# Kernel tuning notes

Measured on AMD Instinct MI355X. Metric: run time of the kernel, lower is better.

Reference implementation:

```python
import jax, jax.numpy as jnp
from jax import lax
import numpy as np

B, S, D_IN = 2048, 512, 5
H, E_DIM, N_EMB, C_CONV = 64, 32, 64, 32
COMMIT = 0.01


def _lstm_params(key, in_dim, hid):
    ks = jax.random.split(key, 4)
    sc = 1.0 / np.sqrt(hid)
    wih = jax.random.uniform(ks[0], (4 * hid, in_dim), minval=-sc, maxval=sc)
    whh = jax.random.uniform(ks[1], (4 * hid, hid), minval=-sc, maxval=sc)
    bih = jax.random.uniform(ks[2], (4 * hid,), minval=-sc, maxval=sc)
    bhh = jax.random.uniform(ks[3], (4 * hid,), minval=-sc, maxval=sc)
    return wih, whh, bih, bhh


def setup_inputs() -> dict:
    key = jax.random.key(0)
    ks = jax.random.split(key, 12)
    inp = {}
    inp['x'] = jax.random.normal(ks[0], (B, S, D_IN), dtype=jnp.float32)
    inp['conv_w'] = jax.random.normal(ks[1], (C_CONV, D_IN, 3)) * 0.2  # OIH
    inp['conv_b'] = jax.random.normal(ks[2], (C_CONV,)) * 0.05
    inp['bn_g'] = jnp.ones((C_CONV,)) + jax.random.normal(ks[3], (C_CONV,)) * 0.05
    inp['bn_b'] = jax.random.normal(ks[4], (C_CONV,)) * 0.05
    inp['bn_m'] = jax.random.normal(ks[5], (C_CONV,)) * 0.1
    inp['bn_v'] = jax.random.uniform(ks[6], (C_CONV,), minval=0.5, maxval=1.5)
    cw = _lstm_params(ks[7], C_CONV, H)
    cw1 = _lstm_params(jax.random.fold_in(ks[7], 1), H, H)
    vw = _lstm_params(ks[8], D_IN, H)
    vw1 = _lstm_params(jax.random.fold_in(ks[8], 1), H, H)
    for pre, p in (('cnn0', cw), ('cnn1', cw1), ('vq0', vw), ('vq1', vw1)):
        inp[pre + '_wih'], inp[pre + '_whh'], inp[pre + '_bih'], inp[pre + '_bhh'] = p
    inp['proj_w'] = jax.random.normal(ks[9], (E_DIM, H)) * (1.0 / np.sqrt(H))
    inp['proj_b'] = jax.random.normal(ks[10], (E_DIM,)) * 0.05
    xav = np.sqrt(6.0 / (N_EMB + E_DIM))
    inp['codebook'] = jax.random.uniform(ks[11], (N_EMB, E_DIM), minval=-xav, maxval=xav)
    return inp


def _lstm_layer(xs, wih, whh, bih, bhh):
    # xs: [S, B, in] -> (ys [S,B,H], h_final [B,H])
    b = xs.shape[1]
    h0 = jnp.zeros((b, H), xs.dtype)
    bias = bih + bhh

    def step(carry, x_t):
        h, c = carry
        gates = x_t @ wih.T + h @ whh.T + bias
        i, f, g, o = jnp.split(gates, 4, axis=-1)
        c = jax.nn.sigmoid(f) * c + jax.nn.sigmoid(i) * jnp.tanh(g)
        h = jax.nn.sigmoid(o) * jnp.tanh(c)
        return (h, c), h

    (h, c), ys = lax.scan(step, (h0, h0), xs)
    return ys, h


def _forward(x, conv_w, conv_b, bn_g, bn_b, bn_m, bn_v,
             cnn0_wih, cnn0_whh, cnn0_bih, cnn0_bhh,
             cnn1_wih, cnn1_whh, cnn1_bih, cnn1_bhh,
             vq0_wih, vq0_whh, vq0_bih, vq0_bhh,
             vq1_wih, vq1_whh, vq1_bih, vq1_bhh,
             proj_w, proj_b, codebook):
    # CNN stream: conv1d(k=3, pad=1) + BN (eval) + ReLU; dropout = identity (eval)
    x_ncw = jnp.transpose(x, (0, 2, 1))  # [B, D_IN, S]
    y = lax.conv_general_dilated(x_ncw, conv_w, (1,), [(1, 1)],
                                 dimension_numbers=('NCH', 'OIH', 'NCH'))
    y = y + conv_b[None, :, None]
    y = (y - bn_m[None, :, None]) * (bn_g / jnp.sqrt(bn_v + 1e-5))[None, :, None] + bn_b[None, :, None]
    y = jax.nn.relu(y)
    y = jnp.transpose(y, (2, 0, 1))  # [S, B, 32] time-major
    ys, _ = _lstm_layer(y, cnn0_wih, cnn0_whh, cnn0_bih, cnn0_bhh)
    _, cnn_features = _lstm_layer(ys, cnn1_wih, cnn1_whh, cnn1_bih, cnn1_bhh)  # [B, H]

    # VQ stream
    xt = jnp.transpose(x, (1, 0, 2))  # [S, B, D_IN]
    ys2, _ = _lstm_layer(xt, vq0_wih, vq0_whh, vq0_bih, vq0_bhh)
    _, vq_hidden = _lstm_layer(ys2, vq1_wih, vq1_whh, vq1_bih, vq1_bhh)  # [B, H]
    vq_proj = vq_hidden @ proj_w.T + proj_b  # [B, E_DIM]

    # Vector quantization
    d = (jnp.sum(vq_proj ** 2, axis=1, keepdims=True)
         + jnp.sum(codebook ** 2, axis=1)
         - 2.0 * vq_proj @ codebook.T)  # [B, N_EMB]
    idx = jnp.argmin(d, axis=1)
    quantized = codebook[idx]  # [B, E_DIM]
    e_loss = jnp.mean((lax.stop_gradient(quantized) - vq_proj) ** 2)
    q_loss = jnp.mean((quantized - lax.stop_gradient(vq_proj)) ** 2)
    vq_loss = q_loss + COMMIT * e_loss
    quantized = vq_proj + lax.stop_gradient(quantized - vq_proj)  # STE
    enc = jax.nn.one_hot(idx, N_EMB, dtype=vq_proj.dtype)
    avg_probs = jnp.mean(enc, axis=0)
    perplexity = jnp.exp(-jnp.sum(avg_probs * jnp.log(avg_probs + 1e-10)))

    combined = jnp.concatenate([cnn_features, quantized], axis=1)  # [B, H+E_DIM]
    return combined, vq_loss, perplexity


def reference(x, conv_w, conv_b, bn_g, bn_b, bn_m, bn_v,
              cnn0_wih, cnn0_whh, cnn0_bih, cnn0_bhh,
              cnn1_wih, cnn1_whh, cnn1_bih, cnn1_bhh,
              vq0_wih, vq0_whh, vq0_bih, vq0_bhh,
              vq1_wih, vq1_whh, vq1_bih, vq1_bhh,
              proj_w, proj_b, codebook):
    combined, vq_loss, perplexity = _forward(
        x, conv_w, conv_b, bn_g, bn_b, bn_m, bn_v,
        cnn0_wih, cnn0_whh, cnn0_bih, cnn0_bhh,
        cnn1_wih, cnn1_whh, cnn1_bih, cnn1_bhh,
        vq0_wih, vq0_whh, vq0_bih, vq0_bhh,
        vq1_wih, vq1_whh, vq1_bih, vq1_bhh,
        proj_w, proj_b, codebook)
    # num_classes=None -> returns (combined, combined, vq_loss, perplexity)
    return combined, combined, vq_loss, perplexity
```

## Files before the change

kernel.cpp:

```cpp
#include <hip/hip_runtime.h>
#include <math.h>
#include <stdint.h>

#define B_TOT 2048
#define SEQ   512
#define DIN   5
#define HID   64
#define EDIM  32
#define NEMB  64
#define BT    16
#define NBLK_STREAM 128
#define COMB  96
#define OUTC  (B_TOT*COMB)

typedef __attribute__((ext_vector_type(8))) _Float16 half8;
typedef __attribute__((ext_vector_type(4))) float float4v;

#if __has_builtin(__builtin_amdgcn_exp2f)
#define FEXP2(x) __builtin_amdgcn_exp2f(x)
#else
#define FEXP2(x) exp2f(x)
#endif
#if __has_builtin(__builtin_amdgcn_rcpf)
#define FRCP(x) __builtin_amdgcn_rcpf(x)
#else
#define FRCP(x) (1.0f/(x))
#endif

#define L2E  1.44269504089f
#define L2E2 2.88539008178f

__device__ __forceinline__ float lstm_cell(float4v a, const float* bp, float& c){
  float ei = FEXP2(fmaf(a[0], -L2E,  bp[0]));
  float ef = FEXP2(fmaf(a[1], -L2E,  bp[1]));
  float eg = FEXP2(fmaf(a[2], -L2E2, bp[2]));
  float eo = FEXP2(fmaf(a[3], -L2E,  bp[3]));
  float Dig = (1.f + ei) * (1.f + eg);
  float Df  = 1.f + ef;
  float rD  = FRCP(Dig * Df);
  float t   = fmaf(-eg, Df, Df);
  c = fmaf(c, Dig, t) * rD;
  float ec = FEXP2(fminf(-L2E2 * c, 126.f));
  return (1.f - ec) * FRCP((1.f + eo) * (1.f + ec));
}

#define MFMA16(a,b,c) __builtin_amdgcn_mfma_f32_16x16x32_f16((a),(b),(c),0,0,0)

#define LOOP_BARRIER() do { \
    asm volatile("s_waitcnt lgkmcnt(0)" ::: "memory"); \
    __builtin_amdgcn_s_barrier(); \
  } while (0)

__global__ __launch_bounds__(1024)
__attribute__((amdgpu_waves_per_eu(4, 4)))
void fused_kernel(const float* __restrict__ xg,
                  const float* __restrict__ conv_w, const float* __restrict__ conv_b,
                  const float* __restrict__ bn_g, const float* __restrict__ bn_b,
                  const float* __restrict__ bn_m, const float* __restrict__ bn_v,
                  const float* __restrict__ cnn0_wih, const float* __restrict__ cnn0_whh,
                  const float* __restrict__ cnn0_bih, const float* __restrict__ cnn0_bhh,
                  const float* __restrict__ cnn1_wih, const float* __restrict__ cnn1_whh,
                  const float* __restrict__ cnn1_bih, const float* __restrict__ cnn1_bhh,
                  const float* __restrict__ vq0_wih, const float* __restrict__ vq0_whh,
                  const float* __restrict__ vq0_bih, const float* __restrict__ vq0_bhh,
                  const float* __restrict__ vq1_wih, const float* __restrict__ vq1_whh,
                  const float* __restrict__ vq1_bih, const float* __restrict__ vq1_bhh,
                  const float* __restrict__ proj_w, const float* __restrict__ proj_b,
                  const float* __restrict__ codebook,
                  float* __restrict__ out, float* __restrict__ ws_f,
                  int* __restrict__ ws_hist, int* __restrict__ ws_cnt)
{
  __shared__ __align__(16) _Float16 ZT[2][5][4][BT][8];
  __shared__ __align__(16) float hfin[BT][HID];
  __shared__ __align__(16) float pbuf[BT][EDIM];
  __shared__ float xwin[4][BT][DIN];

  const int tid  = threadIdx.x;
  const bool is_cnn = (blockIdx.x < NBLK_STREAM);
  const int b0   = (is_cnn ? blockIdx.x : blockIdx.x - NBLK_STREAM) * BT;
  const int w    = tid >> 6;
  const int lane = tid & 63;
  const int n16  = lane & 15;
  const int quad = lane >> 4;
  const int u    = 4*w + quad;

  if (!is_cnn) {
    if (tid < NEMB) atomicExch(&ws_hist[tid], 0);
    else if (tid == NEMB) atomicExch(ws_f, 0.f);
    else if (tid == NEMB+1) atomicExch(ws_cnt, 0);
  }

  const float* wih0 = is_cnn ? cnn0_wih : vq0_wih;
  const float* whh0 = is_cnn ? cnn0_whh : vq0_whh;
  const float* bih0 = is_cnn ? cnn0_bih : vq0_bih;
  const float* bhh0 = is_cnn ? cnn0_bhh : vq0_bhh;
  const float* wih1 = is_cnn ? cnn1_wih : vq1_wih;
  const float* whh1 = is_cnn ? cnn1_whh : vq1_whh;
  const float* bih1 = is_cnn ? cnn1_bih : vq1_bih;
  const float* bhh1 = is_cnn ? cnn1_bhh : vq1_bhh;

  const int orow = 64*(n16 & 3) + 4*w + (n16 >> 2);
  half8 Ah0[3], Ah1[4];
#pragma unroll
  for (int kt = 0; kt < 3; ++kt) {
    half8 vh;
#pragma unroll
    for (int j = 0; j < 8; ++j) {
      const int g = kt*32 + quad*8 + j;
      float wv;
      if (is_cnn) wv = (g < 32) ? wih0[orow*32 + g] : whh0[orow*64 + (g-32)];
      else        wv = (g < 5) ? wih0[orow*5 + g] : (g < 32 ? 0.f : whh0[orow*64 + (g-32)]);
      vh[j] = (_Float16)wv;
    }
    Ah0[kt] = vh;
  }
#pragma unroll
  for (int kt = 0; kt < 4; ++kt) {
    half8 vh;
#pragma unroll
    for (int j = 0; j < 8; ++j) {
      const int g = kt*32 + quad*8 + j;
      float wv = (g < 64) ? wih1[orow*64 + g] : whh1[orow*64 + (g-64)];
      vh[j] = (_Float16)wv;
    }
    Ah1[kt] = vh;
  }

  float bp0[4], bp1[4];
#pragma unroll
  for (int r = 0; r < 4; ++r) {
    const float k = (r == 2) ? L2E2 : L2E;
    bp0[r] = -k * (bih0[64*r + u] + bhh0[64*r + u]);
    bp1[r] = -k * (bih1[64*r + u] + bhh1[64*r + u]);
  }
  const float4v zero4 = {0.f, 0.f, 0.f, 0.f};

  float wr[16];
#pragma unroll
  for (int i = 0; i < 16; ++i) wr[i] = 0.f;
  if (is_cnn && tid < 512) {
    const int cc = tid >> 4;
    float s = bn_g[cc] * rsqrtf(bn_v[cc] + 1e-5f);
#pragma unroll
    for (int i = 0; i < 5; ++i)
#pragma unroll
      for (int tau = 0; tau < 3; ++tau)
        wr[tau*5 + i] = conv_w[cc*15 + i*3 + tau] * s;
    wr[15] = (conv_b[cc] - bn_m[cc]) * s + bn_b[cc];
  }

  for (int i2 = tid; i2 < 2*5*4*BT*8/2; i2 += 1024) ((uint32_t*)ZT)[i2] = 0;

  const int xn = tid / 5, xi = tid % 5;
  float xpref = 0.f;

  #define ZB(b) ((_Float16*)(&ZT[(b)][0][0][0][0]))
  #define ZIDX(tile,k32,n) (((tile)*4 + (((k32)>>3)&3))*(BT*8) + (n)*8 + ((k32)&7))

  if (is_cnn) {
    if (tid < BT*DIN) {
#pragma unroll
      for (int j = 0; j < 4; ++j)
        xwin[j][xn][xi] = xg[((size_t)(b0+xn)*SEQ + j)*DIN + xi];
    }
  }
  __syncthreads();

  if (is_cnn) {
    if (tid < 512) {
      const int cc = tid >> 4, cn = tid & 15;
      float s = wr[15];
#pragma unroll
      for (int i = 0; i < 5; ++i)
        s += wr[5+i]*xwin[0][cn][i] + wr[10+i]*xwin[1][cn][i];
      s = fmaxf(s, 0.f);
      ZB(1)[ZIDX(0, cc, cn)] = (_Float16)s;
    }
  } else {
    if (tid < BT*DIN) {
      float xv = xg[((size_t)(b0+xn)*SEQ + 0)*DIN + xi];
      ZB(1)[ZIDX(0, xi, xn)] = (_Float16)xv;
    }
  }
  __syncthreads();

  float c0 = 0.f, c1 = 0.f, h1v = 0.f;
  float convA = 0.f, convB = 0.f;
  {
    half8 bt0 = *(const half8*)&ZT[1][0][quad][n16][0];
    half8 bt1 = *(const half8*)&ZT[1][1][quad][n16][0];
    half8 bt2 = *(const half8*)&ZT[1][2][quad][n16][0];
    float4v a0 = MFMA16(Ah0[0], bt0, zero4);
    a0 = MFMA16(Ah0[1], bt1, a0);
    a0 = MFMA16(Ah0[2], bt2, a0);
    float h0 = lstm_cell(a0, bp0, c0);
    ZB(0)[ZIDX(1 + (u>>5), u & 31, n16)] = (_Float16)h0;
  }
  if (is_cnn) {
    if (tid < 512) {
      const int cc = tid >> 4, cn = tid & 15;
      float s = wr[15];
      float r01 = 0.f, r12 = 0.f, r02 = 0.f;
#pragma unroll
      for (int i = 0; i < 5; ++i) {
        const float x0v = xwin[0][cn][i], x1v = xwin[1][cn][i], x2v = xwin[2][cn][i];
        s   += wr[i]*x0v + wr[5+i]*x1v + wr[10+i]*x2v;
        r01 = fmaf(wr[i],   x1v, r01);
        r12 = fmaf(wr[5+i], x2v, r12);
        r02 = fmaf(wr[i],   x2v, r02);
      }
      s = fmaxf(s, 0.f);
      ZB(0)[ZIDX(0, cc, cn)] = (_Float16)s;
      convA = wr[15] + r01 + r12;
      convB = wr[15] + r02;
    }
    if (tid < BT*DIN) xpref = xg[((size_t)(b0+xn)*SEQ + 4)*DIN + xi];
  } else {
    if (tid < BT*DIN) {
      float xv = xg[((size_t)(b0+xn)*SEQ + 1)*DIN + xi];
      ZB(0)[ZIDX(0, xi, xn)] = (_Float16)xv;
      xpref = xg[((size_t)(b0+xn)*SEQ + 2)*DIN + xi];
    }
  }
  __syncthreads();

#pragma unroll 2
  for (int t = 0; t < SEQ; ++t) {
    const int rb = t & 1, wrb = rb ^ 1;
    half8 bt0 = *(const half8*)&ZT[rb][0][quad][n16][0];
    half8 bt1 = *(const half8*)&ZT[rb][1][quad][n16][0];
    half8 bt2 = *(const half8*)&ZT[rb][2][quad][n16][0];
    half8 bt3 = *(const half8*)&ZT[rb][3][quad][n16][0];
    half8 bt4 = *(const half8*)&ZT[rb][4][quad][n16][0];
    float4v a1 = MFMA16(Ah1[0], bt1, zero4);
    a1 = MFMA16(Ah1[1], bt2, a1);
    a1 = MFMA16(Ah1[2], bt3, a1);
    a1 = MFMA16(Ah1[3], bt4, a1);
    float4v a0 = MFMA16(Ah0[0], bt0, zero4);
    a0 = MFMA16(Ah0[1], bt1, a0);
    a0 = MFMA16(Ah0[2], bt2, a0);

    __builtin_amdgcn_s_setprio(1);
    {
      float h1 = lstm_cell(a1, bp1, c1);
      ZB(wrb)[ZIDX(3 + (u>>5), u & 31, n16)] = (_Float16)h1;
      if (is_cnn) h1v = h1;
      else if (t == SEQ-1) hfin[n16][u] = h1;
    }
    {
      float h0 = lstm_cell(a0, bp0, c0);
      ZB(wrb)[ZIDX(1 + (u>>5), u & 31, n16)] = (_Float16)h0;
    }
    if (is_cnn) {
      if (tid < 512) {
        const float* x3 = xwin[(t+3)&3][tid & 15];
        float r0 = 0.f, r1 = 0.f, r2 = 0.f;
#pragma unroll
        for (int i = 0; i < 5; ++i) {
          const float xv = x3[i];
          r0 = fmaf(wr[i],    xv, r0);
          r1 = fmaf(wr[5+i],  xv, r1);
          r2 = fmaf(wr[10+i], xv, r2);
        }
        float y = fmaxf(convA + r2, 0.f);
        ZB(wrb)[ZIDX(0, tid >> 4, tid & 15)] = (_Float16)y;
        convA = convB + r1;
        convB = wr[15] + r0;
      }
      if (tid < BT*DIN) {
        xwin[t & 3][xn][xi] = xpref;
        const int tq = t + 5;
        xpref = (tq < SEQ) ? xg[((size_t)(b0+xn)*SEQ + tq)*DIN + xi] : 0.f;
      }
    } else {
      if (tid < BT*DIN) {
        ZB(wrb)[ZIDX(0, xi, xn)] = (_Float16)xpref;
        const int tq = t + 3;
        xpref = (tq < SEQ) ? xg[((size_t)(b0+xn)*SEQ + tq)*DIN + xi] : 0.f;
      }
    }
    __builtin_amdgcn_s_setprio(0);
    LOOP_BARRIER();
  }

  if (is_cnn) {
    const size_t gb = (size_t)(b0 + n16);
    out[gb*COMB + u]        = h1v;
    out[OUTC + gb*COMB + u] = h1v;
  } else {
    if (tid < 512) {
      const int pn = tid >> 5, pe = tid & 31;
      float s = proj_b[pe];
      const float* pw = proj_w + pe*HID;
#pragma unroll
      for (int k = 0; k < HID; ++k) s += hfin[pn][k] * pw[k];
      pbuf[pn][pe] = s;
    }
    __syncthreads();
    {
      const int bb = w;
      const int nn = lane;
      const float* cbn = codebook + nn*EDIM;
      float d = 0.f;
#pragma unroll
      for (int k = 0; k < EDIM; ++k) { float df = pbuf[bb][k] - cbn[k]; d += df*df; }
      int bi = nn;
#pragma unroll
      for (int off = 32; off > 0; off >>= 1) {
        float od = __shfl_down(d, off, 64);
        int   oi = __shfl_down(bi, off, 64);
        if (od < d || (od == d && oi < bi)) { d = od; bi = oi; }
      }
      bi = __shfl(bi, 0, 64);
      float lv = 0.f;
      if (nn < EDIM) {
        float q = codebook[bi*EDIM + nn];
        const size_t gb = (size_t)(b0 + bb);
        out[gb*COMB + HID + nn]        = q;
        out[OUTC + gb*COMB + HID + nn] = q;
        float df = q - pbuf[bb][nn];
        lv = df*df;
      }
#pragma unroll
      for (int off = 32; off > 0; off >>= 1) lv += __shfl_down(lv, off, 64);
      if (nn == 0) { atomicAdd(ws_f, lv); atomicAdd(&ws_hist[bi], 1); }
    }
    if (w == 0) {
      __threadfence();
      int c = 0;
      if (lane == 0) c = atomicAdd(ws_cnt, 1);
      c = __shfl(c, 0, 64);
      if (c == NBLK_STREAM - 1) {
        __threadfence();
        int hv = atomicAdd(&ws_hist[lane], 0);
        float p = (float)hv * (1.0f / (float)B_TOT);
        float e = -p * logf(p + 1e-10f);
#pragma unroll
        for (int off = 32; off > 0; off >>= 1) e += __shfl_down(e, off, 64);
        if (lane == 0) {
          float wf = atomicAdd(ws_f, 0.0f);
          float mse = wf * (1.0f / (float)(B_TOT * EDIM));
          out[2*OUTC + 0] = mse * 1.01f;
          out[2*OUTC + 1] = expf(e);
        }
      }
    }
  }
}

extern "C" void kernel_launch(void* const* d_in, const int* in_sizes, int n_in,
                              void* d_out, int out_size, void* d_ws, size_t ws_size,
                              hipStream_t stream) {
  const float* x        = (const float*)d_in[0];
  const float* conv_w   = (const float*)d_in[1];
  const float* conv_b   = (const float*)d_in[2];
  const float* bn_g     = (const float*)d_in[3];
  const float* bn_b     = (const float*)d_in[4];
  const float* bn_m     = (const float*)d_in[5];
  const float* bn_v     = (const float*)d_in[6];
  const float* cnn0_wih = (const float*)d_in[7];
  const float* cnn0_whh = (const float*)d_in[8];
  const float* cnn0_bih = (const float*)d_in[9];
  const float* cnn0_bhh = (const float*)d_in[10];
  const float* cnn1_wih = (const float*)d_in[11];
  const float* cnn1_whh = (const float*)d_in[12];
  const float* cnn1_bih = (const float*)d_in[13];
  const float* cnn1_bhh = (const float*)d_in[14];
  const float* vq0_wih  = (const float*)d_in[15];
  const float* vq0_whh  = (const float*)d_in[16];
  const float* vq0_bih  = (const float*)d_in[17];
  const float* vq0_bhh  = (const float*)d_in[18];
  const float* vq1_wih  = (const float*)d_in[19];
  const float* vq1_whh  = (const float*)d_in[20];
  const float* vq1_bih  = (const float*)d_in[21];
  const float* vq1_bhh  = (const float*)d_in[22];
  const float* proj_w   = (const float*)d_in[23];
  const float* proj_b   = (const float*)d_in[24];
  const float* codebook = (const float*)d_in[25];

  float* out     = (float*)d_out;
  float* ws_f    = (float*)d_ws;
  int*   ws_hist = (int*)d_ws + 16;
  int*   ws_cnt  = (int*)d_ws + 88;

  hipLaunchKernelGGL(fused_kernel, dim3(2*NBLK_STREAM), dim3(1024), 0, stream,
                     x, conv_w, conv_b, bn_g, bn_b, bn_m, bn_v,
                     cnn0_wih, cnn0_whh, cnn0_bih, cnn0_bhh,
                     cnn1_wih, cnn1_whh, cnn1_bih, cnn1_bhh,
                     vq0_wih, vq0_whh, vq0_bih, vq0_bhh,
                     vq1_wih, vq1_whh, vq1_bih, vq1_bhh,
                     proj_w, proj_b, codebook, out, ws_f, ws_hist, ws_cnt);
}
```

Before: 523.9 us.

## Split LSTM layers across wave groups, each wave computing two gate tiles

Waves 0-7 now handle only layer 0 and waves 8-15 only layer 1, with each wave computing two 16-row M-tiles (units uA and uA+32) instead of one tile of both layers. This keeps each wave's MFMA chain and LSTM cell work uniform and lets the two independent tile accumulators interleave to hide MFMA latency. Layer-0 waves run three MFMAs per tile and layer-1 waves four, so the per-step load is unequal and the barrier waits on the slower layer-1 group. Register use per wave changes because each wave now holds two tiles of weights.

```diff
diff --git a/kernel.cpp b/kernel.cpp
--- a/kernel.cpp
+++ b/kernel.cpp
@@ -82,7 +82,9 @@
   const int lane = tid & 63;
   const int n16  = lane & 15;
   const int quad = lane >> 4;
-  const int u    = 4*w + quad;
+  const bool isL1 = (w >= 8);
+  const int wm   = w & 7;
+  const int uA   = 4*wm + quad;
 
   if (!is_cnn) {
     if (tid < NEMB) atomicExch(&ws_hist[tid], 0);
@@ -90,48 +92,51 @@
     else if (tid == NEMB+1) atomicExch(ws_cnt, 0);
   }
 
-  const float* wih0 = is_cnn ? cnn0_wih : vq0_wih;
-  const float* whh0 = is_cnn ? cnn0_whh : vq0_whh;
-  const float* bih0 = is_cnn ? cnn0_bih : vq0_bih;
-  const float* bhh0 = is_cnn ? cnn0_bhh : vq0_bhh;
-  const float* wih1 = is_cnn ? cnn1_wih : vq1_wih;
-  const float* whh1 = is_cnn ? cnn1_whh : vq1_whh;
-  const float* bih1 = is_cnn ? cnn1_bih : vq1_bih;
-  const float* bhh1 = is_cnn ? cnn1_bhh : vq1_bhh;
-
-  const int orow = 64*(n16 & 3) + 4*w + (n16 >> 2);
-  half8 Ah0[3], Ah1[4];
-#pragma unroll
-  for (int kt = 0; kt < 3; ++kt) {
-    half8 vh;
-#pragma unroll
-    for (int j = 0; j < 8; ++j) {
-      const int g = kt*32 + quad*8 + j;
-      float wv;
-      if (is_cnn) wv = (g < 32) ? wih0[orow*32 + g] : whh0[orow*64 + (g-32)];
-      else        wv = (g < 5) ? wih0[orow*5 + g] : (g < 32 ? 0.f : whh0[orow*64 + (g-32)]);
-      vh[j] = (_Float16)wv;
-    }
-    Ah0[kt] = vh;
-  }
-#pragma unroll
-  for (int kt = 0; kt < 4; ++kt) {
-    half8 vh;
-#pragma unroll
-    for (int j = 0; j < 8; ++j) {
-      const int g = kt*32 + quad*8 + j;
-      float wv = (g < 64) ? wih1[orow*64 + g] : whh1[orow*64 + (g-64)];
-      vh[j] = (_Float16)wv;
-    }
-    Ah1[kt] = vh;
-  }
-
-  float bp0[4], bp1[4];
-#pragma unroll
-  for (int r = 0; r < 4; ++r) {
-    const float k = (r == 2) ? L2E2 : L2E;
-    bp0[r] = -k * (bih0[64*r + u] + bhh0[64*r + u]);
-    bp1[r] = -k * (bih1[64*r + u] + bhh1[64*r + u]);
+  const float* wih = is_cnn ? (isL1 ? cnn1_wih : cnn0_wih) : (isL1 ? vq1_wih : vq0_wih);
+  const float* whh = is_cnn ? (isL1 ? cnn1_whh : cnn0_whh) : (isL1 ? vq1_whh : vq0_whh);
+  const float* bih = is_cnn ? (isL1 ? cnn1_bih : cnn0_bih) : (isL1 ? vq1_bih : vq0_bih);
+  const float* bhh = is_cnn ? (isL1 ? cnn1_bhh : cnn0_bhh) : (isL1 ? vq1_bhh : vq0_bhh);
+
+  half8 Ah[2][4];
+  float bp[2][4];
+#pragma unroll
+  for (int mt = 0; mt < 2; ++mt) {
+    const int T = wm + 8*mt;
+    const int orow = 64*(n16 & 3) + 4*T + (n16 >> 2);
+    if (!isL1) {
+#pragma unroll
+      for (int kt = 0; kt < 3; ++kt) {
+        half8 vh;
+#pragma unroll
+        for (int j = 0; j < 8; ++j) {
+          const int g = kt*32 + quad*8 + j;
+          float wv;
+          if (is_cnn) wv = (g < 32) ? wih[orow*32 + g] : whh[orow*64 + (g-32)];
+          else        wv = (g < 5) ? wih[orow*5 + g] : (g < 32 ? 0.f : whh[orow*64 + (g-32)]);
+          vh[j] = (_Float16)wv;
+        }
+        Ah[mt][kt] = vh;
+      }
+      Ah[mt][3] = half8{};
+    } else {
+#pragma unroll
+      for (int kt = 0; kt < 4; ++kt) {
+        half8 vh;
+#pragma unroll
+        for (int j = 0; j < 8; ++j) {
+          const int g = kt*32 + quad*8 + j;
+          float wv = (g < 64) ? wih[orow*64 + g] : whh[orow*64 + (g-64)];
+          vh[j] = (_Float16)wv;
+        }
+        Ah[mt][kt] = vh;
+      }
+    }
+    const int u = uA + 32*mt;
+#pragma unroll
+    for (int r = 0; r < 4; ++r) {
+      const float k = (r == 2) ? L2E2 : L2E;
+      bp[mt][r] = -k * (bih[64*r + u] + bhh[64*r + u]);
+    }
   }
   const float4v zero4 = {0.f, 0.f, 0.f, 0.f};
 
@@ -184,17 +189,21 @@
   }
   __syncthreads();
 
-  float c0 = 0.f, c1 = 0.f, h1v = 0.f;
+  float c[2] = {0.f, 0.f};
+  float h1v[2] = {0.f, 0.f};
   float convA = 0.f, convB = 0.f;
-  {
+  if (!isL1) {
     half8 bt0 = *(const half8*)&ZT[1][0][quad][n16][0];
     half8 bt1 = *(const half8*)&ZT[1][1][quad][n16][0];
     half8 bt2 = *(const half8*)&ZT[1][2][quad][n16][0];
-    float4v a0 = MFMA16(Ah0[0], bt0, zero4);
-    a0 = MFMA16(Ah0[1], bt1, a0);
-    a0 = MFMA16(Ah0[2], bt2, a0);
-    float h0 = lstm_cell(a0, bp0, c0);
-    ZB(0)[ZIDX(1 + (u>>5), u & 31, n16)] = (_Float16)h0;
+#pragma unroll
+    for (int mt = 0; mt < 2; ++mt) {
+      float4v a0 = MFMA16(Ah[mt][0], bt0, zero4);
+      a0 = MFMA16(Ah[mt][1], bt1, a0);
+      a0 = MFMA16(Ah[mt][2], bt2, a0);
+      float h0 = lstm_cell(a0, bp[mt], c[mt]);
+      ZB(0)[ZIDX(1 + mt, uA, n16)] = (_Float16)h0;
+    }
   }
   if (is_cnn) {
     if (tid < 512) {
@@ -227,29 +236,38 @@
 #pragma unroll 2
   for (int t = 0; t < SEQ; ++t) {
     const int rb = t & 1, wrb = rb ^ 1;
-    half8 bt0 = *(const half8*)&ZT[rb][0][quad][n16][0];
-    half8 bt1 = *(const half8*)&ZT[rb][1][quad][n16][0];
-    half8 bt2 = *(const half8*)&ZT[rb][2][quad][n16][0];
-    half8 bt3 = *(const half8*)&ZT[rb][3][quad][n16][0];
-    half8 bt4 = *(const half8*)&ZT[rb][4][quad][n16][0];
-    float4v a1 = MFMA16(Ah1[0], bt1, zero4);
-    a1 = MFMA16(Ah1[1], bt2, a1);
-    a1 = MFMA16(Ah1[2], bt3, a1);
-    a1 = MFMA16(Ah1[3], bt4, a1);
-    float4v a0 = MFMA16(Ah0[0], bt0, zero4);
-    a0 = MFMA16(Ah0[1], bt1, a0);
-    a0 = MFMA16(Ah0[2], bt2, a0);
+    half8 btA, btB, btC, btD;
+    if (isL1) {
+      btA = *(const half8*)&ZT[rb][1][quad][n16][0];
+      btB = *(const half8*)&ZT[rb][2][quad][n16][0];
+      btC = *(const half8*)&ZT[rb][3][quad][n16][0];
+      btD = *(const half8*)&ZT[rb][4][quad][n16][0];
+    } else {
+      btA = *(const half8*)&ZT[rb][0][quad][n16][0];
+      btB = *(const half8*)&ZT[rb][1][quad][n16][0];
+      btC = *(const half8*)&ZT[rb][2][quad][n16][0];
+    }
+    float4v a[2];
+#pragma unroll
+    for (int mt = 0; mt < 2; ++mt) a[mt] = MFMA16(Ah[mt][0], btA, zero4);
+#pragma unroll
+    for (int mt = 0; mt < 2; ++mt) a[mt] = MFMA16(Ah[mt][1], btB, a[mt]);
+#pragma unroll
+    for (int mt = 0; mt < 2; ++mt) a[mt] = MFMA16(Ah[mt][2], btC, a[mt]);
+    if (isL1) {
+#pragma unroll
+      for (int mt = 0; mt < 2; ++mt) a[mt] = MFMA16(Ah[mt][3], btD, a[mt]);
+    }
 
     __builtin_amdgcn_s_setprio(1);
-    {
-      float h1 = lstm_cell(a1, bp1, c1);
-      ZB(wrb)[ZIDX(3 + (u>>5), u & 31, n16)] = (_Float16)h1;
-      if (is_cnn) h1v = h1;
-      else if (t == SEQ-1) hfin[n16][u] = h1;
-    }
-    {
-      float h0 = lstm_cell(a0, bp0, c0);
-      ZB(wrb)[ZIDX(1 + (u>>5), u & 31, n16)] = (_Float16)h0;
+#pragma unroll
+    for (int mt = 0; mt < 2; ++mt) {
+      float h = lstm_cell(a[mt], bp[mt], c[mt]);
+      ZB(wrb)[ZIDX((isL1 ? 3 : 1) + mt, uA, n16)] = (_Float16)h;
+      if (isL1) {
+        if (is_cnn) h1v[mt] = h;
+        else if (t == SEQ-1) hfin[n16][uA + 32*mt] = h;
+      }
     }
     if (is_cnn) {
       if (tid < 512) {
@@ -284,9 +302,13 @@
   }
 
   if (is_cnn) {
-    const size_t gb = (size_t)(b0 + n16);
-    out[gb*COMB + u]        = h1v;
-    out[OUTC + gb*COMB + u] = h1v;
+    if (isL1) {
+      const size_t gb = (size_t)(b0 + n16);
+      out[gb*COMB + uA]             = h1v[0];
+      out[OUTC + gb*COMB + uA]      = h1v[0];
+      out[gb*COMB + uA + 32]        = h1v[1];
+      out[OUTC + gb*COMB + uA + 32] = h1v[1];
+    }
   } else {
     if (tid < 512) {
       const int pn = tid >> 5, pe = tid & 31;
@@ -327,10 +349,10 @@
     }
     if (w == 0) {
       __threadfence();
-      int c = 0;
-      if (lane == 0) c = atomicAdd(ws_cnt, 1);
-      c = __shfl(c, 0, 64);
-      if (c == NBLK_STREAM - 1) {
+      int cc2 = 0;
+      if (lane == 0) cc2 = atomicAdd(ws_cnt, 1);
+      cc2 = __shfl(cc2, 0, 64);
+      if (cc2 == NBLK_STREAM - 1) {
         __threadfence();
         int hv = atomicAdd(&ws_hist[lane], 0);
         float p = (float)hv * (1.0f / (float)B_TOT);
```

Measured after the change: 588.6 us. 12.3% more time.
